# Kernel optimization log

Measured on AMD Instinct MI355X. Metric: run time of the kernel, lower is better.

Reference implementation:

```python
import jax, jax.numpy as jnp
import numpy as np

T, N, F, L, A = 4, 16, 6, 1024, 21  # genomes, tiles, frames, tile length, alphabet
K, U = 20, 256                      # profile width, number of profiles


def setup_inputs() -> dict:
    key = jax.random.key(0)
    k1, k2 = jax.random.split(key)
    X = jax.random.uniform(k1, (T, N, F, L, A), dtype=jnp.float32)
    Q = jnp.ones((A,), dtype=jnp.float32) / A  # uniform background distribution
    # P_logit ~ log(Q) + N(0, 4) as in _getRandomProfiles
    P_logit = (jnp.log(Q)[None, :, None]
               + 4.0 * jax.random.normal(k2, (K, A, U), dtype=jnp.float32))
    return {"X": X, "P_logit": P_logit, "Q": Q}


def reference(X, P_logit, Q):
    # SpecificProfile.call(X) -> (S, R, Z)
    Tb, Nb, Fb, Lb, Ab = X.shape
    k, _, units = P_logit.shape
    # getR: P = softmax(P_logit, axis=1); R = log(max(P / Q, epsilon))
    P = jax.nn.softmax(P_logit, axis=1)                    # [k, A, U]
    epsilon = jnp.mean(Q)                                   # exp(-log(1/mean(Q)))
    R = jnp.log(jnp.maximum(P / Q[None, :, None], epsilon))  # [k, A, U]
    # getZ: conv2d over (length, alphabet) spatial dims, VALID padding
    Xr = X.reshape(Tb * Nb * Fb, Lb, Ab, 1)                 # NHWC
    Kr = R[:, :, None, :]                                   # HWIO: [k, A, 1, U]
    Z = jax.lax.conv_general_dilated(
        Xr, Kr, window_strides=(1, 1), padding='VALID',
        dimension_numbers=('NHWC', 'HWIO', 'NHWC'))          # [TNF, L-k+1, 1, U]
    Z = Z.reshape(Tb, Nb, Fb, Lb - k + 1, units)            # [T, N, F, P, U]
    S = jnp.max(Z, axis=(2, 3))                             # [T, N, U]
    return S, R, Z
```

## Files before the change

kernel.cpp:

```cpp
#include <hip/hip_runtime.h>
#include <hip/hip_bf16.h>
#include <math.h>

#define T_ 4
#define N_ 16
#define F_ 6
#define L_ 1024
#define A_ 21
#define K_ 20
#define U_ 256
#define LOUT 1005
#define NIMG 384
#define SZ_S (T_*N_*U_)
#define SZ_R (K_*A_*U_)

#define XPR 24
#define XROWS 1056
#define NSTEP 15
#define RT_SHORTS (NSTEP * U_ * 32)
#define XCHUNKS 14

typedef __attribute__((ext_vector_type(8))) short short8;
typedef __attribute__((ext_vector_type(4))) float f32x4;

__device__ __forceinline__ unsigned short f2bf(float f) {
  unsigned int u = __float_as_uint(f);
  u += 0x7FFFu + ((u >> 16) & 1u);
  return (unsigned short)(u >> 16);
}

__device__ __forceinline__ void atomicMaxF(float* addr, float val) {
  if (val >= 0.f) atomicMax((int*)addr, __float_as_int(val));
  else            atomicMin((unsigned int*)addr, __float_as_uint(val));
}

__device__ __forceinline__ void gload_lds16(const void* g, void* l) {
  __builtin_amdgcn_global_load_lds(
      (const __attribute__((address_space(1))) void*)g,
      (__attribute__((address_space(3))) void*)l, 16, 0, 0);
}

__global__ void prep_kernel(const float* __restrict__ P_logit,
                            const float* __restrict__ Q,
                            float* __restrict__ out,
                            unsigned short* __restrict__ Rt) {
  int tid = blockIdx.x * blockDim.x + threadIdx.x;
  if (tid < SZ_S) out[tid] = -INFINITY;
  if (tid >= K_ * U_) return;
  int k = tid / U_;
  int u = tid - k * U_;
  const float* pl = P_logit + (size_t)k * A_ * U_ + u;
  float v[A_];
  float m = -INFINITY;
#pragma unroll
  for (int a = 0; a < A_; ++a) { v[a] = pl[(size_t)a * U_]; m = fmaxf(m, v[a]); }
  float s = 0.f;
#pragma unroll
  for (int a = 0; a < A_; ++a) { v[a] = expf(v[a] - m); s += v[a]; }
  float qs = 0.f;
#pragma unroll
  for (int a = 0; a < A_; ++a) qs += Q[a];
  float eps = qs * (1.0f / A_);
  float invs = 1.f / s;
  float* Rout = out + SZ_S;
#pragma unroll
  for (int a = 0; a < A_; ++a) {
    float r = logf(fmaxf(v[a] * invs / Q[a], eps));
    Rout[(size_t)(k * A_ + a) * U_ + u] = r;
    int sl = k * XPR + a;
    Rt[(size_t)(sl >> 5) * (U_ * 32) + u * 32 + (sl & 31)] = f2bf(r);
  }
#pragma unroll
  for (int a = A_; a < XPR; ++a) {
    int sl = k * XPR + a;
    Rt[(size_t)(sl >> 5) * (U_ * 32) + u * 32 + (sl & 31)] = 0;
  }
}

__global__ void xconv_kernel(const float* __restrict__ X,
                             unsigned int* __restrict__ Xp32) {
  int t = blockIdx.x * blockDim.x + threadIdx.x;
  if (t >= NIMG * XROWS * 12) return;
  int w  = t % 12;
  int rl = t / 12;
  int row = rl % XROWS;
  int n   = rl / XROWS;
  int c0 = w * 2;
  float v0 = 0.f, v1 = 0.f;
  if (row < L_) {
    const float* xr = X + ((size_t)n * L_ + row) * A_;
    if (c0 < A_)     v0 = xr[c0];
    if (c0 + 1 < A_) v1 = xr[c0 + 1];
  }
  unsigned int o = (unsigned int)f2bf(v0) | ((unsigned int)f2bf(v1) << 16);
  Xp32[(size_t)rl * 12 + w] = o;
}

__global__ __launch_bounds__(256, 2) void conv_kernel(
    const unsigned short* __restrict__ Xp,
    const unsigned short* __restrict__ Rt,
    float* __restrict__ out) {
  __shared__ __align__(16) unsigned short lds_x[XCHUNKS * 512];
  __shared__ __align__(16) unsigned short lds_r[4][4][2048];

  const int n  = blockIdx.z;
  const int l0 = blockIdx.y * 256;
  const int u0 = blockIdx.x * 128;
  const int wid  = threadIdx.x >> 6;
  const int lane = threadIdx.x & 63;
  const int wl = wid >> 1;
  const int wu = wid & 1;

  const char* xsrc = (const char*)Xp + ((size_t)n * XROWS + l0) * (XPR * 2);
  const char* rsrc = (const char*)Rt + (size_t)u0 * 64 + wu * 4096;
  char* rdst = (char*)&lds_r[wid][0][0];

#define STAGE(KK)                                                            \
  {                                                                          \
    _Pragma("unroll")                                                        \
    for (int c = 0; c < 4; ++c)                                              \
      gload_lds16(rsrc + (size_t)(KK) * (U_ * 64) + c * 1024 + lane * 16,    \
                  rdst + ((KK) & 3) * 4096 + c * 1024);                      \
  }

  for (int c = wid; c < XCHUNKS; c += 4)
    gload_lds16(xsrc + c * 1024 + lane * 16, (char*)lds_x + c * 1024);
  STAGE(0) STAGE(1) STAGE(2)
  asm volatile("s_waitcnt vmcnt(12)" ::: "memory");
  __builtin_amdgcn_s_barrier();

  const int fl = lane & 15;
  const int fj = lane >> 4;

  f32x4 acc[4][8];
#pragma unroll
  for (int ut = 0; ut < 4; ++ut)
#pragma unroll
    for (int lt = 0; lt < 8; ++lt)
      acc[ut][lt] = (f32x4){0.f, 0.f, 0.f, 0.f};

  const unsigned short* xb = lds_x + (wl * 128 + fl) * XPR + (fj << 3);
  const unsigned short* rbw =
      (const unsigned short*)rdst + fl * 32 + (fj << 3);

#define READ_FRAGS(KK, X8, R4)                                               \
  {                                                                          \
    const unsigned short* rb = rbw + ((KK) & 3) * 2048;                      \
    _Pragma("unroll")                                                        \
    for (int lt = 0; lt < 8; ++lt)                                           \
      (X8)[lt] = *(const short8*)(xb + lt * (16 * XPR) + (KK) * 32);         \
    _Pragma("unroll")                                                        \
    for (int ut = 0; ut < 4; ++ut)                                           \
      (R4)[ut] = *(const short8*)(rb + ut * (16 * 32));                      \
  }

#define MFMA32(R4, X8)                                                       \
  {                                                                          \
    __builtin_amdgcn_s_setprio(1);                                           \
    _Pragma("unroll")                                                        \
    for (int ut = 0; ut < 4; ++ut)                                           \
      _Pragma("unroll")                                                      \
      for (int lt = 0; lt < 8; ++lt)                                         \
        acc[ut][lt] = __builtin_amdgcn_mfma_f32_16x16x32_bf16(               \
            (R4)[ut], (X8)[lt], acc[ut][lt], 0, 0, 0);                       \
    __builtin_amdgcn_s_setprio(0);                                           \
  }

  short8 fx[2][8], fr[2][4];
  asm volatile("s_waitcnt vmcnt(8)" ::: "memory");
  READ_FRAGS(0, fx[0], fr[0])

#pragma unroll
  for (int k = 0; k < NSTEP; ++k) {
    const int cb = k & 1, nb = cb ^ 1;
    if (k + 3 < NSTEP) STAGE(k + 3)
    if (k + 1 < NSTEP) {
      if (k <= NSTEP - 4)      asm volatile("s_waitcnt vmcnt(8)" ::: "memory");
      else if (k == NSTEP - 3) asm volatile("s_waitcnt vmcnt(4)" ::: "memory");
      else                     asm volatile("s_waitcnt vmcnt(0)" ::: "memory");
      READ_FRAGS(k + 1, fx[nb], fr[nb])
    }
    MFMA32(fr[cb], fx[cb])
  }

#undef READ_FRAGS
#undef MFMA32
#undef STAGE

  float* Z = out + SZ_S + SZ_R;
  const int ug = fj << 2;
  float pmax[4][4];
#pragma unroll
  for (int ut = 0; ut < 4; ++ut)
#pragma unroll
    for (int r = 0; r < 4; ++r) pmax[ut][r] = -INFINITY;

#pragma unroll
  for (int lt = 0; lt < 8; ++lt) {
    const int l = l0 + wl * 128 + lt * 16 + fl;
    if (l < LOUT) {
      float* zrow = Z + ((size_t)n * LOUT + l) * U_ + u0 + wu * 64 + ug;
#pragma unroll
      for (int ut = 0; ut < 4; ++ut) {
        f32x4 v = acc[ut][lt];
        *(f32x4*)(zrow + ut * 16) = v;
#pragma unroll
        for (int r = 0; r < 4; ++r) pmax[ut][r] = fmaxf(pmax[ut][r], v[r]);
      }
    }
  }

#pragma unroll
  for (int off = 1; off < 16; off <<= 1)
#pragma unroll
    for (int ut = 0; ut < 4; ++ut)
#pragma unroll
      for (int r = 0; r < 4; ++r)
        pmax[ut][r] = fmaxf(pmax[ut][r], __shfl_xor(pmax[ut][r], off));

  if (fl == 0) {
    const int tn = n / F_;
    float* Sp = out + (size_t)tn * U_ + u0 + wu * 64 + ug;
#pragma unroll
    for (int ut = 0; ut < 4; ++ut)
#pragma unroll
      for (int r = 0; r < 4; ++r)
        atomicMaxF(Sp + ut * 16 + r, pmax[ut][r]);
  }
}

extern "C" void kernel_launch(void* const* d_in, const int* in_sizes, int n_in,
                              void* d_out, int out_size, void* d_ws, size_t ws_size,
                              hipStream_t stream) {
  const float* X       = (const float*)d_in[0];
  const float* P_logit = (const float*)d_in[1];
  const float* Q       = (const float*)d_in[2];
  float* out = (float*)d_out;

  unsigned short* Rt = (unsigned short*)d_ws;
  unsigned short* Xp = (unsigned short*)((char*)d_ws + 262144);

  hipLaunchKernelGGL(prep_kernel, dim3(64), dim3(256), 0, stream,
                     P_logit, Q, out, Rt);
  int xthreads = NIMG * XROWS * 12;
  hipLaunchKernelGGL(xconv_kernel, dim3((xthreads + 255) / 256), dim3(256),
                     0, stream, X, (unsigned int*)Xp);
  dim3 grid(2, 4, NIMG);
  hipLaunchKernelGGL(conv_kernel, grid, dim3(256), 0, stream, Xp, Rt, out);
}
```

Before: 148.4 us.

## Switch conv to 32x32x16 MFMA tiles and merge prep kernels into one launch

The conv kernel now uses 32x32x16 bf16 MFMA instructions with 2x4 accumulator tiles in place of 16x16x32 with 4x8 tiles. This halves the number of MFMA issues and changes how fragments are read from LDS. The R weight layout is reshuffled in the prep step to match the new fragment shape, and the epilogue's stores, shuffle max-reduction and atomics are rewritten for the 32-row layout. The profile-prep and X-conversion kernels are fused into one launch to save a launch gap. The main risks are different LDS bank-conflict behaviour and a longer shuffle reduction chain.

```diff
diff --git a/kernel.cpp b/kernel.cpp
--- a/kernel.cpp
+++ b/kernel.cpp
@@ -17,11 +17,12 @@
 #define XPR 24
 #define XROWS 1056
 #define NSTEP 15
-#define RT_SHORTS (NSTEP * U_ * 32)
 #define XCHUNKS 14
+
 
 typedef __attribute__((ext_vector_type(8))) short short8;
 typedef __attribute__((ext_vector_type(4))) float f32x4;
+typedef __attribute__((ext_vector_type(16))) float f32x16;
 
 __device__ __forceinline__ unsigned short f2bf(float f) {
   unsigned int u = __float_as_uint(f);
@@ -40,60 +41,65 @@
       (__attribute__((address_space(3))) void*)l, 16, 0, 0);
 }
 
-__global__ void prep_kernel(const float* __restrict__ P_logit,
-                            const float* __restrict__ Q,
-                            float* __restrict__ out,
-                            unsigned short* __restrict__ Rt) {
-  int tid = blockIdx.x * blockDim.x + threadIdx.x;
-  if (tid < SZ_S) out[tid] = -INFINITY;
-  if (tid >= K_ * U_) return;
-  int k = tid / U_;
-  int u = tid - k * U_;
-  const float* pl = P_logit + (size_t)k * A_ * U_ + u;
-  float v[A_];
-  float m = -INFINITY;
-#pragma unroll
-  for (int a = 0; a < A_; ++a) { v[a] = pl[(size_t)a * U_]; m = fmaxf(m, v[a]); }
-  float s = 0.f;
-#pragma unroll
-  for (int a = 0; a < A_; ++a) { v[a] = expf(v[a] - m); s += v[a]; }
-  float qs = 0.f;
-#pragma unroll
-  for (int a = 0; a < A_; ++a) qs += Q[a];
-  float eps = qs * (1.0f / A_);
-  float invs = 1.f / s;
-  float* Rout = out + SZ_S;
-#pragma unroll
-  for (int a = 0; a < A_; ++a) {
-    float r = logf(fmaxf(v[a] * invs / Q[a], eps));
-    Rout[(size_t)(k * A_ + a) * U_ + u] = r;
-    int sl = k * XPR + a;
-    Rt[(size_t)(sl >> 5) * (U_ * 32) + u * 32 + (sl & 31)] = f2bf(r);
-  }
-#pragma unroll
-  for (int a = A_; a < XPR; ++a) {
-    int sl = k * XPR + a;
-    Rt[(size_t)(sl >> 5) * (U_ * 32) + u * 32 + (sl & 31)] = 0;
-  }
-}
-
-__global__ void xconv_kernel(const float* __restrict__ X,
+__global__ void xprep_kernel(const float* __restrict__ X,
+                             const float* __restrict__ P_logit,
+                             const float* __restrict__ Q,
+                             float* __restrict__ out,
+                             unsigned short* __restrict__ Rt,
                              unsigned int* __restrict__ Xp32) {
   int t = blockIdx.x * blockDim.x + threadIdx.x;
-  if (t >= NIMG * XROWS * 12) return;
-  int w  = t % 12;
-  int rl = t / 12;
-  int row = rl % XROWS;
-  int n   = rl / XROWS;
-  int c0 = w * 2;
-  float v0 = 0.f, v1 = 0.f;
-  if (row < L_) {
-    const float* xr = X + ((size_t)n * L_ + row) * A_;
-    if (c0 < A_)     v0 = xr[c0];
-    if (c0 + 1 < A_) v1 = xr[c0 + 1];
-  }
-  unsigned int o = (unsigned int)f2bf(v0) | ((unsigned int)f2bf(v1) << 16);
-  Xp32[(size_t)rl * 12 + w] = o;
+  if (t < SZ_S) out[t] = -INFINITY;
+
+  if (t < K_ * U_) {
+    int k = t / U_;
+    int u = t - k * U_;
+    const float* pl = P_logit + (size_t)k * A_ * U_ + u;
+    float v[A_];
+    float m = -INFINITY;
+#pragma unroll
+    for (int a = 0; a < A_; ++a) { v[a] = pl[(size_t)a * U_]; m = fmaxf(m, v[a]); }
+    float s = 0.f;
+#pragma unroll
+    for (int a = 0; a < A_; ++a) { v[a] = expf(v[a] - m); s += v[a]; }
+    float qs = 0.f;
+#pragma unroll
+    for (int a = 0; a < A_; ++a) qs += Q[a];
+    float eps = qs * (1.0f / A_);
+    float invs = 1.f / s;
+    float* Rout = out + SZ_S;
+    const int H  = u >> 6;
+    const int ut = (u >> 5) & 1;
+    const int r  = u & 31;
+#pragma unroll
+    for (int a = 0; a < XPR; ++a) {
+      float rv = 0.f;
+      if (a < A_) {
+        rv = logf(fmaxf(v[a] * invs / Q[a], eps));
+        Rout[(size_t)(k * A_ + a) * U_ + u] = rv;
+      }
+      int sl = k * XPR + a;
+      int b = sl >> 5, s5 = sl & 31;
+      int h = s5 >> 4, q = (s5 >> 3) & 1, j = s5 & 7;
+      Rt[(size_t)b * 8192 + H * 2048 + (ut * 2 + h) * 512 + (r * 2 + q) * 8 + j]
+          = (a < A_) ? f2bf(rv) : 0;
+    }
+  }
+
+  if (t < NIMG * XROWS * 12) {
+    int w  = t % 12;
+    int rl = t / 12;
+    int row = rl % XROWS;
+    int n   = rl / XROWS;
+    int c0 = w * 2;
+    float v0 = 0.f, v1 = 0.f;
+    if (row < L_) {
+      const float* xr = X + ((size_t)n * L_ + row) * A_;
+      if (c0 < A_)     v0 = xr[c0];
+      if (c0 + 1 < A_) v1 = xr[c0 + 1];
+    }
+    unsigned int o = (unsigned int)f2bf(v0) | ((unsigned int)f2bf(v1) << 16);
+    Xp32[(size_t)rl * 12 + w] = o;
+  }
 }
 
 __global__ __launch_bounds__(256, 2) void conv_kernel(
@@ -112,14 +118,15 @@
   const int wu = wid & 1;
 
   const char* xsrc = (const char*)Xp + ((size_t)n * XROWS + l0) * (XPR * 2);
-  const char* rsrc = (const char*)Rt + (size_t)u0 * 64 + wu * 4096;
+  const int H = (u0 >> 6) + wu;
+  const char* rsrc = (const char*)Rt + (size_t)H * 4096;
   char* rdst = (char*)&lds_r[wid][0][0];
 
 #define STAGE(KK)                                                            \
   {                                                                          \
     _Pragma("unroll")                                                        \
     for (int c = 0; c < 4; ++c)                                              \
-      gload_lds16(rsrc + (size_t)(KK) * (U_ * 64) + c * 1024 + lane * 16,    \
+      gload_lds16(rsrc + (size_t)(KK) * 16384 + c * 1024 + lane * 16,        \
                   rdst + ((KK) & 3) * 4096 + c * 1024);                      \
   }
 
@@ -129,44 +136,52 @@
   asm volatile("s_waitcnt vmcnt(12)" ::: "memory");
   __builtin_amdgcn_s_barrier();
 
-  const int fl = lane & 15;
-  const int fj = lane >> 4;
-
-  f32x4 acc[4][8];
-#pragma unroll
-  for (int ut = 0; ut < 4; ++ut)
-#pragma unroll
-    for (int lt = 0; lt < 8; ++lt)
-      acc[ut][lt] = (f32x4){0.f, 0.f, 0.f, 0.f};
-
-  const unsigned short* xb = lds_x + (wl * 128 + fl) * XPR + (fj << 3);
+  const int r32 = lane & 31;
+  const int hi  = lane >> 5;
+
+  f32x16 acc[2][4];
+#pragma unroll
+  for (int ut = 0; ut < 2; ++ut)
+#pragma unroll
+    for (int lt = 0; lt < 4; ++lt)
+#pragma unroll
+      for (int i = 0; i < 16; ++i) acc[ut][lt][i] = 0.f;
+
+  const unsigned short* xb = lds_x + (wl * 128 + r32) * XPR + hi * 8;
   const unsigned short* rbw =
-      (const unsigned short*)rdst + fl * 32 + (fj << 3);
-
-#define READ_FRAGS(KK, X8, R4)                                               \
+      (const unsigned short*)rdst + r32 * 16 + hi * 8;
+
+#define READ_FRAGS(KK, X8, R8)                                               \
   {                                                                          \
-    const unsigned short* rb = rbw + ((KK) & 3) * 2048;                      \
-    _Pragma("unroll")                                                        \
-    for (int lt = 0; lt < 8; ++lt)                                           \
-      (X8)[lt] = *(const short8*)(xb + lt * (16 * XPR) + (KK) * 32);         \
-    _Pragma("unroll")                                                        \
-    for (int ut = 0; ut < 4; ++ut)                                           \
-      (R4)[ut] = *(const short8*)(rb + ut * (16 * 32));                      \
-  }
-
-#define MFMA32(R4, X8)                                                       \
+    _Pragma("unroll")                                                        \
+    for (int lt = 0; lt < 4; ++lt)                                           \
+      _Pragma("unroll")                                                      \
+      for (int h = 0; h < 2; ++h)                                            \
+        (X8)[lt][h] =                                                        \
+            *(const short8*)(xb + lt * (32 * XPR) + (KK) * 32 + h * 16);     \
+    _Pragma("unroll")                                                        \
+    for (int ut = 0; ut < 2; ++ut)                                           \
+      _Pragma("unroll")                                                      \
+      for (int h = 0; h < 2; ++h)                                            \
+        (R8)[ut][h] = *(const short8*)(rbw + ((KK) & 3) * 2048 +             \
+                                       (ut * 2 + h) * 512);                  \
+  }
+
+#define MFMA16(R8, X8)                                                       \
   {                                                                          \
     __builtin_amdgcn_s_setprio(1);                                           \
     _Pragma("unroll")                                                        \
-    for (int ut = 0; ut < 4; ++ut)                                           \
+    for (int h = 0; h < 2; ++h)                                              \
       _Pragma("unroll")                                                      \
-      for (int lt = 0; lt < 8; ++lt)                                         \
-        acc[ut][lt] = __builtin_amdgcn_mfma_f32_16x16x32_bf16(               \
-            (R4)[ut], (X8)[lt], acc[ut][lt], 0, 0, 0);                       \
+      for (int ut = 0; ut < 2; ++ut)                                         \
+        _Pragma("unroll")                                                    \
+        for (int lt = 0; lt < 4; ++lt)                                       \
+          acc[ut][lt] = __builtin_amdgcn_mfma_f32_32x32x16_bf16(             \
+              (R8)[ut][h], (X8)[lt][h], acc[ut][lt], 0, 0, 0);               \
     __builtin_amdgcn_s_setprio(0);                                           \
   }
 
-  short8 fx[2][8], fr[2][4];
+  short8 fx[2][4][2], fr[2][2][2];
   asm volatile("s_waitcnt vmcnt(8)" ::: "memory");
   READ_FRAGS(0, fx[0], fr[0])
 
@@ -180,52 +195,63 @@
       else                     asm volatile("s_waitcnt vmcnt(0)" ::: "memory");
       READ_FRAGS(k + 1, fx[nb], fr[nb])
     }
-    MFMA32(fr[cb], fx[cb])
+    MFMA16(fr[cb], fx[cb])
   }
 
 #undef READ_FRAGS
-#undef MFMA32
+#undef MFMA16
 #undef STAGE
 
   float* Z = out + SZ_S + SZ_R;
-  const int ug = fj << 2;
-  float pmax[4][4];
-#pragma unroll
-  for (int ut = 0; ut < 4; ++ut)
-#pragma unroll
-    for (int r = 0; r < 4; ++r) pmax[ut][r] = -INFINITY;
-
-#pragma unroll
-  for (int lt = 0; lt < 8; ++lt) {
-    const int l = l0 + wl * 128 + lt * 16 + fl;
+  f32x4 pm[2][4];
+#pragma unroll
+  for (int ut = 0; ut < 2; ++ut)
+#pragma unroll
+    for (int rq = 0; rq < 4; ++rq)
+#pragma unroll
+      for (int j = 0; j < 4; ++j) pm[ut][rq][j] = -INFINITY;
+
+#pragma unroll
+  for (int lt = 0; lt < 4; ++lt) {
+    const int l = l0 + wl * 128 + lt * 32 + r32;
     if (l < LOUT) {
-      float* zrow = Z + ((size_t)n * LOUT + l) * U_ + u0 + wu * 64 + ug;
-#pragma unroll
-      for (int ut = 0; ut < 4; ++ut) {
-        f32x4 v = acc[ut][lt];
-        *(f32x4*)(zrow + ut * 16) = v;
-#pragma unroll
-        for (int r = 0; r < 4; ++r) pmax[ut][r] = fmaxf(pmax[ut][r], v[r]);
+#pragma unroll
+      for (int ut = 0; ut < 2; ++ut) {
+        float* zrow = Z + ((size_t)n * LOUT + l) * U_ + u0 + wu * 64 +
+                      ut * 32 + hi * 4;
+#pragma unroll
+        for (int rq = 0; rq < 4; ++rq) {
+          f32x4 v;
+#pragma unroll
+          for (int j = 0; j < 4; ++j) v[j] = acc[ut][lt][4 * rq + j];
+          *(f32x4*)(zrow + 8 * rq) = v;
+#pragma unroll
+          for (int j = 0; j < 4; ++j) pm[ut][rq][j] = fmaxf(pm[ut][rq][j], v[j]);
+        }
       }
     }
   }
 
 #pragma unroll
-  for (int off = 1; off < 16; off <<= 1)
-#pragma unroll
-    for (int ut = 0; ut < 4; ++ut)
-#pragma unroll
-      for (int r = 0; r < 4; ++r)
-        pmax[ut][r] = fmaxf(pmax[ut][r], __shfl_xor(pmax[ut][r], off));
-
-  if (fl == 0) {
+  for (int off = 1; off < 32; off <<= 1)
+#pragma unroll
+    for (int ut = 0; ut < 2; ++ut)
+#pragma unroll
+      for (int rq = 0; rq < 4; ++rq)
+#pragma unroll
+        for (int j = 0; j < 4; ++j)
+          pm[ut][rq][j] = fmaxf(pm[ut][rq][j], __shfl_xor(pm[ut][rq][j], off));
+
+  if (r32 == 0) {
     const int tn = n / F_;
-    float* Sp = out + (size_t)tn * U_ + u0 + wu * 64 + ug;
-#pragma unroll
-    for (int ut = 0; ut < 4; ++ut)
-#pragma unroll
-      for (int r = 0; r < 4; ++r)
-        atomicMaxF(Sp + ut * 16 + r, pmax[ut][r]);
+    float* Sp = out + (size_t)tn * U_ + u0 + wu * 64 + hi * 4;
+#pragma unroll
+    for (int ut = 0; ut < 2; ++ut)
+#pragma unroll
+      for (int rq = 0; rq < 4; ++rq)
+#pragma unroll
+        for (int j = 0; j < 4; ++j)
+          atomicMaxF(Sp + ut * 32 + 8 * rq + j, pm[ut][rq][j]);
   }
 }
 
@@ -240,11 +266,9 @@
   unsigned short* Rt = (unsigned short*)d_ws;
   unsigned short* Xp = (unsigned short*)((char*)d_ws + 262144);
 
-  hipLaunchKernelGGL(prep_kernel, dim3(64), dim3(256), 0, stream,
-                     P_logit, Q, out, Rt);
   int xthreads = NIMG * XROWS * 12;
-  hipLaunchKernelGGL(xconv_kernel, dim3((xthreads + 255) / 256), dim3(256),
-                     0, stream, X, (unsigned int*)Xp);
+  hipLaunchKernelGGL(xprep_kernel, dim3((xthreads + 255) / 256), dim3(256),
+                     0, stream, X, P_logit, Q, out, Rt, (unsigned int*)Xp);
   dim3 grid(2, 4, NIMG);
   hipLaunchKernelGGL(conv_kernel, grid, dim3(256), 0, stream, Xp, Rt, out);
 }
```

Result: slower. 196.9 us (+32.7%).
